# Performance work log

Measured on AMD Instinct MI355X. Metric: run time of the kernel, lower is better.

## Reference

```python
import jax, jax.numpy as jnp
import numpy as np

WINDOW_SIZE = 11
SIGMA = 1.5
C1 = 0.01 ** 2
C2 = 0.03 ** 2
LAMBDA_DSSIM = 0.2


def _gaussian_window(channel):
    x = jnp.arange(WINDOW_SIZE, dtype=jnp.float32)
    g = jnp.exp(-((x - WINDOW_SIZE // 2) ** 2) / (2.0 * SIGMA ** 2))
    g = g / g.sum()
    w2d = jnp.outer(g, g)  # [ws, ws]
    # depthwise kernel: [O=C, I=1, ws, ws]
    return jnp.broadcast_to(w2d[None, None], (channel, 1, WINDOW_SIZE, WINDOW_SIZE))


def _dwconv(x, window, channel):
    # x: [1, C, H, W]; same padding ws//2, depthwise (groups=C)
    pad = WINDOW_SIZE // 2
    return jax.lax.conv_general_dilated(
        x, window,
        window_strides=(1, 1),
        padding=((pad, pad), (pad, pad)),
        dimension_numbers=("NCHW", "OIHW", "NCHW"),
        feature_group_count=channel,
    )


def _ssim_mean(img1, img2):
    # img1, img2: [C, H, W]
    channel = img1.shape[0]
    window = _gaussian_window(channel).astype(img1.dtype)
    a = img1[None]  # [1, C, H, W]
    b = img2[None]

    mu1 = _dwconv(a, window, channel)
    mu2 = _dwconv(b, window, channel)
    mu1_sq = mu1 * mu1
    mu2_sq = mu2 * mu2
    mu1_mu2 = mu1 * mu2
    sigma1_sq = _dwconv(a * a, window, channel) - mu1_sq
    sigma2_sq = _dwconv(b * b, window, channel) - mu2_sq
    sigma12 = _dwconv(a * b, window, channel) - mu1_mu2

    ssim_map = ((2 * mu1_mu2 + C1) * (2 * sigma12 + C2)) / (
        (mu1_sq + mu2_sq + C1) * (sigma1_sq + sigma2_sq + C2))
    return ssim_map.mean()


def setup_inputs() -> dict:
    key = jax.random.key(0)
    k1, k2 = jax.random.split(key)
    shape = (3, 2160, 3840)
    pred = jax.random.uniform(k1, shape, dtype=jnp.float32)
    target = jax.random.uniform(k2, shape, dtype=jnp.float32)
    return {"pred": pred, "target": target}


def reference(pred, target):
    l1 = jnp.abs(pred - target).mean()
    ssim_val = _ssim_mean(pred, target)
    return (1.0 - LAMBDA_DSSIM) * l1 + LAMBDA_DSSIM * (1.0 - ssim_val)
```

## Files before the change

kernel.cpp:

```cpp
#include <hip/hip_runtime.h>
#include <math.h>

#define WSZ 11
#define PAD 5
#define TX 32
#define TY 24
#define NY 6
#define IY (TY + 2*PAD)
#define RX 4
#define NTASK0 (IY * 8)
#define NTASK1 (TY * 8)
#define SEG (RX + 2*PAD)
#define RY 3
#define SA 33
#define SB 35

typedef float v2f __attribute__((ext_vector_type(2)));

struct W11 { float w[WSZ]; };

__global__ __launch_bounds__(256, 4) void ssim_l1_kernel(
    const float* __restrict__ pred, const float* __restrict__ targ,
    W11 wt, float2* __restrict__ partials)
{
    constexpr int H = 2160, W = 3840;
    __shared__ float4 sHA[IY][SA];
    __shared__ float  sHB[IY][SB];

    const int c    = blockIdx.z;
    const int gx0  = blockIdx.x * TX;
    const int base = blockIdx.y * (TY * NY);
    const size_t plane = (size_t)H * W;
    const float* p = pred + (size_t)c * plane;
    const float* t = targ + (size_t)c * plane;

    const int tid = threadIdx.x;
    v2f loss_acc = {0.f, 0.f};
    const float C1v = 0.0001f, C2v = 0.0009f;

    const int oxB  = tid & 31;
    const int oy0B = (tid >> 5) * RY;
    const bool xfast = (blockIdx.x >= 1) && (blockIdx.x <= (W / TX) - 2);

    for (int s = 0; s < NY; ++s) {
        if (s > 0) {
            for (int i = tid; i < 2 * PAD * TX; i += 256) {
                const int dr = i >> 5, cc = i & 31;
                sHA[dr][cc] = sHA[dr + TY][cc];
                sHB[dr][cc] = sHB[dr + TY][cc];
            }
            __syncthreads();
        }

        const int ntask  = (s == 0) ? NTASK0 : NTASK1;
        const int rowoff = (s == 0) ? 0 : 2 * PAD;
        const int gyA    = base + TY * s - PAD;
        for (int task = tid; task < ntask; task += 256) {
            const int r  = task >> 3;
            const int cx = task & 7;
            const int rr = rowoff + r;
            const int gy = gyA + rr;
            const int gxs = gx0 + cx * RX - PAD;
            const bool rowok   = (gy >= 0) && (gy < H);
            const bool own_row = (gy >= base) && (gy < base + TY * NY);

            float4 P[5], T[5];
            if (rowok && xfast) {
                const float4* p4 = (const float4*)(p + (size_t)gy * W + (gxs - 3));
                const float4* t4 = (const float4*)(t + (size_t)gy * W + (gxs - 3));
                #pragma unroll
                for (int i = 0; i < 5; ++i) { P[i] = p4[i]; T[i] = t4[i]; }
            } else if (rowok) {
                const size_t rowoff2 = (size_t)gy * W;
                #pragma unroll
                for (int i = 0; i < 5; ++i) {
                    float pe[4], te[4];
                    #pragma unroll
                    for (int q = 0; q < 4; ++q) {
                        int gx = gxs - 3 + 4 * i + q;
                        bool ok = (gx >= 0) && (gx < W);
                        pe[q] = ok ? p[rowoff2 + gx] : 0.f;
                        te[q] = ok ? t[rowoff2 + gx] : 0.f;
                    }
                    P[i] = make_float4(pe[0], pe[1], pe[2], pe[3]);
                    T[i] = make_float4(te[0], te[1], te[2], te[3]);
                }
            } else {
                #pragma unroll
                for (int i = 0; i < 5; ++i) {
                    P[i] = make_float4(0.f, 0.f, 0.f, 0.f);
                    T[i] = make_float4(0.f, 0.f, 0.f, 0.f);
                }
            }

            v2f h_ab[RX], h_sq[RX];
            float h_pt[RX];
            #pragma unroll
            for (int j = 0; j < RX; ++j) {
                h_ab[j] = (v2f){0.f, 0.f};
                h_sq[j] = (v2f){0.f, 0.f};
                h_pt[j] = 0.f;
            }
            #pragma unroll
            for (int e = 0; e < SEG; ++e) {
                const int ii = (e + 3) >> 2, qq = (e + 3) & 3;
                const float pe = (qq == 0) ? P[ii].x : (qq == 1) ? P[ii].y
                                : (qq == 2) ? P[ii].z : P[ii].w;
                const float te = (qq == 0) ? T[ii].x : (qq == 1) ? T[ii].y
                                : (qq == 2) ? T[ii].z : T[ii].w;
                v2f vab; vab.x = pe; vab.y = te;
                const v2f vsq = vab * vab;
                const float pt = pe * te;
                #pragma unroll
                for (int j = 0; j < RX; ++j) {
                    const int k = e - j;
                    if (k >= 0 && k < WSZ) {
                        const float wv = wt.w[k];
                        h_ab[j] += wv * vab;
                        h_sq[j] += wv * vsq;
                        h_pt[j] += wv * pt;
                    }
                }
                if (e >= PAD && e < PAD + RX && own_row)
                    loss_acc.y += fabsf(pe - te);
            }
            const int xb = cx * RX;
            #pragma unroll
            for (int j = 0; j < RX; ++j) {
                sHA[rr][xb + j] = make_float4(h_ab[j].x, h_ab[j].y,
                                              h_sq[j].x, h_sq[j].y);
                sHB[rr][xb + j] = h_pt[j];
            }
        }
        __syncthreads();

        {
            v2f mu[RY], sq[RY];
            float sp[RY];
            #pragma unroll
            for (int j = 0; j < RY; ++j) {
                mu[j] = (v2f){0.f, 0.f};
                sq[j] = (v2f){0.f, 0.f};
                sp[j] = 0.f;
            }
            #pragma unroll
            for (int k = 0; k < RY + 2 * PAD; ++k) {
                const float4 f = sHA[oy0B + k][oxB];
                const float  g = sHB[oy0B + k][oxB];
                v2f fab; fab.x = f.x; fab.y = f.y;
                v2f fsq; fsq.x = f.z; fsq.y = f.w;
                #pragma unroll
                for (int j = 0; j < RY; ++j) {
                    const int kk = k - j;
                    if (kk >= 0 && kk < WSZ) {
                        const float wv = wt.w[kk];
                        mu[j] += wv * fab;
                        sq[j] += wv * fsq;
                        sp[j] += wv * g;
                    }
                }
            }
            #pragma unroll
            for (int j = 0; j < RY; ++j) {
                const float m1 = mu[j].x, m2 = mu[j].y;
                const float mu1s = m1 * m1;
                const float mu2s = m2 * m2;
                const float m12  = m1 * m2;
                const float num = (2.f * m12 + C1v) * (2.f * (sp[j] - m12) + C2v);
                const float den = (mu1s + mu2s + C1v)
                                * ((sq[j].x - mu1s) + (sq[j].y - mu2s) + C2v);
                loss_acc.x += num * __builtin_amdgcn_rcpf(den);
            }
        }
        __syncthreads();
    }

    #pragma unroll
    for (int off = 32; off > 0; off >>= 1) {
        loss_acc.x += __shfl_down(loss_acc.x, off, 64);
        loss_acc.y += __shfl_down(loss_acc.y, off, 64);
    }
    __shared__ float red[2][4];
    const int lane = tid & 63;
    const int wid  = tid >> 6;
    if (lane == 0) { red[0][wid] = loss_acc.x; red[1][wid] = loss_acc.y; }
    __syncthreads();
    if (tid == 0) {
        const float sv = red[0][0] + red[0][1] + red[0][2] + red[0][3];
        const float lv = red[1][0] + red[1][1] + red[1][2] + red[1][3];
        const int bid = (blockIdx.z * gridDim.y + blockIdx.y) * gridDim.x + blockIdx.x;
        partials[bid] = make_float2(sv, lv);
    }
}

__global__ __launch_bounds__(256) void finalize_kernel(
    const float2* __restrict__ partials, int n,
    float* __restrict__ out, double invN)
{
    const int tid = threadIdx.x;
    double s = 0.0, l = 0.0;
    for (int i = tid; i < n; i += 256) {
        float2 v = partials[i];
        s += (double)v.x;
        l += (double)v.y;
    }
    #pragma unroll
    for (int off = 32; off > 0; off >>= 1) {
        s += __shfl_down(s, off, 64);
        l += __shfl_down(l, off, 64);
    }
    __shared__ double rs[4], rl[4];
    const int lane = tid & 63, wid = tid >> 6;
    if (lane == 0) { rs[wid] = s; rl[wid] = l; }
    __syncthreads();
    if (tid == 0) {
        const double st = rs[0] + rs[1] + rs[2] + rs[3];
        const double lt = rl[0] + rl[1] + rl[2] + rl[3];
        out[0] = (float)(0.8 * lt * invN + 0.2 * (1.0 - st * invN));
    }
}

extern "C" void kernel_launch(void* const* d_in, const int* in_sizes, int n_in,
                              void* d_out, int out_size, void* d_ws, size_t ws_size,
                              hipStream_t stream)
{
    const float* pred = (const float*)d_in[0];
    const float* targ = (const float*)d_in[1];
    float* out = (float*)d_out;
    float2* partials = (float2*)d_ws;

    const int C = 3, H = 2160, W = 3840;

    W11 wt;
    double g[WSZ], sg = 0.0;
    for (int i = 0; i < WSZ; ++i) {
        double d = (double)i - (WSZ / 2);
        g[i] = exp(-(d * d) / (2.0 * 1.5 * 1.5));
        sg += g[i];
    }
    for (int i = 0; i < WSZ; ++i) wt.w[i] = (float)(g[i] / sg);

    dim3 grid(W / TX, H / (TY * NY), C);
    ssim_l1_kernel<<<grid, 256, 0, stream>>>(pred, targ, wt, partials);

    const int nblocks = (W / TX) * (H / (TY * NY)) * C;
    double invN = 1.0 / ((double)C * (double)H * (double)W);
    finalize_kernel<<<1, 256, 0, stream>>>(partials, nblocks, out, invN);
}
```

Baseline: 274.8 us.

## Reformulate SSIM statistics in sum/difference basis to drop fifth filtered channel

Filters s=p+t and d=p-t along with s^2 and d^2 rather than p, t, p^2, t^2 and p*t. The SSIM numerator and denominator are rebuilt from these four sums, which removes the fifth convolved quantity, the separate sHB shared-memory array, its halo copies and its loads. The result is fewer FMAs and less LDS traffic per pixel. The cost is a possible loss of accuracy from cancellation when the products are recovered as differences of squares.

```diff
diff --git a/kernel.cpp b/kernel.cpp
--- a/kernel.cpp
+++ b/kernel.cpp
@@ -13,7 +13,6 @@
 #define SEG (RX + 2*PAD)
 #define RY 3
 #define SA 33
-#define SB 35
 
 typedef float v2f __attribute__((ext_vector_type(2)));
 
@@ -25,7 +24,6 @@
 {
     constexpr int H = 2160, W = 3840;
     __shared__ float4 sHA[IY][SA];
-    __shared__ float  sHB[IY][SB];
 
     const int c    = blockIdx.z;
     const int gx0  = blockIdx.x * TX;
@@ -47,7 +45,6 @@
             for (int i = tid; i < 2 * PAD * TX; i += 256) {
                 const int dr = i >> 5, cc = i & 31;
                 sHA[dr][cc] = sHA[dr + TY][cc];
-                sHB[dr][cc] = sHB[dr + TY][cc];
             }
             __syncthreads();
         }
@@ -93,13 +90,11 @@
                 }
             }
 
-            v2f h_ab[RX], h_sq[RX];
-            float h_pt[RX];
+            v2f h_sd[RX], h_qq[RX];
             #pragma unroll
             for (int j = 0; j < RX; ++j) {
-                h_ab[j] = (v2f){0.f, 0.f};
-                h_sq[j] = (v2f){0.f, 0.f};
-                h_pt[j] = 0.f;
+                h_sd[j] = (v2f){0.f, 0.f};
+                h_qq[j] = (v2f){0.f, 0.f};
             }
             #pragma unroll
             for (int e = 0; e < SEG; ++e) {
@@ -108,68 +103,59 @@
                                 : (qq == 2) ? P[ii].z : P[ii].w;
                 const float te = (qq == 0) ? T[ii].x : (qq == 1) ? T[ii].y
                                 : (qq == 2) ? T[ii].z : T[ii].w;
-                v2f vab; vab.x = pe; vab.y = te;
-                const v2f vsq = vab * vab;
-                const float pt = pe * te;
+                v2f vsd; vsd.x = pe + te; vsd.y = pe - te;
+                const v2f vsq = vsd * vsd;
                 #pragma unroll
                 for (int j = 0; j < RX; ++j) {
                     const int k = e - j;
                     if (k >= 0 && k < WSZ) {
                         const float wv = wt.w[k];
-                        h_ab[j] += wv * vab;
-                        h_sq[j] += wv * vsq;
-                        h_pt[j] += wv * pt;
+                        h_sd[j] += wv * vsd;
+                        h_qq[j] += wv * vsq;
                     }
                 }
                 if (e >= PAD && e < PAD + RX && own_row)
-                    loss_acc.y += fabsf(pe - te);
+                    loss_acc.y += fabsf(vsd.y);
             }
             const int xb = cx * RX;
             #pragma unroll
-            for (int j = 0; j < RX; ++j) {
-                sHA[rr][xb + j] = make_float4(h_ab[j].x, h_ab[j].y,
-                                              h_sq[j].x, h_sq[j].y);
-                sHB[rr][xb + j] = h_pt[j];
-            }
+            for (int j = 0; j < RX; ++j)
+                sHA[rr][xb + j] = make_float4(h_sd[j].x, h_sd[j].y,
+                                              h_qq[j].x, h_qq[j].y);
         }
         __syncthreads();
 
         {
-            v2f mu[RY], sq[RY];
-            float sp[RY];
+            v2f mu[RY], qq[RY];
             #pragma unroll
             for (int j = 0; j < RY; ++j) {
                 mu[j] = (v2f){0.f, 0.f};
-                sq[j] = (v2f){0.f, 0.f};
-                sp[j] = 0.f;
+                qq[j] = (v2f){0.f, 0.f};
             }
             #pragma unroll
             for (int k = 0; k < RY + 2 * PAD; ++k) {
                 const float4 f = sHA[oy0B + k][oxB];
-                const float  g = sHB[oy0B + k][oxB];
-                v2f fab; fab.x = f.x; fab.y = f.y;
+                v2f fsd; fsd.x = f.x; fsd.y = f.y;
                 v2f fsq; fsq.x = f.z; fsq.y = f.w;
                 #pragma unroll
                 for (int j = 0; j < RY; ++j) {
                     const int kk = k - j;
                     if (kk >= 0 && kk < WSZ) {
                         const float wv = wt.w[kk];
-                        mu[j] += wv * fab;
-                        sq[j] += wv * fsq;
-                        sp[j] += wv * g;
+                        mu[j] += wv * fsd;
+                        qq[j] += wv * fsq;
                     }
                 }
             }
             #pragma unroll
             for (int j = 0; j < RY; ++j) {
-                const float m1 = mu[j].x, m2 = mu[j].y;
-                const float mu1s = m1 * m1;
-                const float mu2s = m2 * m2;
-                const float m12  = m1 * m2;
-                const float num = (2.f * m12 + C1v) * (2.f * (sp[j] - m12) + C2v);
-                const float den = (mu1s + mu2s + C1v)
-                                * ((sq[j].x - mu1s) + (sq[j].y - mu2s) + C2v);
-                loss_acc.x += num * __builtin_amdgcn_rcpf(den);
+                const v2f musq = mu[j] * mu[j];
+                const v2f rr2  = qq[j] - musq;
+                const float a  = 0.5f * (musq.x - musq.y) + C1v;
+                const float b  = 0.5f * (rr2.x - rr2.y) + C2v;
+                const float cden = 0.5f * (musq.x + musq.y) + C1v;
+                const float dden = 0.5f * (rr2.x + rr2.y) + C2v;
+                loss_acc.x += (a * b) * __builtin_amdgcn_rcpf(cden * dden);
             }
         }
         __syncthreads();
```

New measurement: 246.8 us. 10.2% less time.
